# Kernel tuning notes

Hardware: AMD Instinct MI355X
Metric: run time of the kernel (lower is better)

Reference implementation:

```python
import jax, jax.numpy as jnp
import numpy as np

D_EMBED = 1024
D_HEAD = 128


def setup_inputs() -> dict:
    key = jax.random.key(0)
    kx, kq, kk, kv = jax.random.split(key, 4)
    x = jax.random.normal(kx, (4, 4096, D_EMBED), dtype=jnp.float32)
    # nn.Linear(d_embed, d_head, bias=False) weights, stored [out, in] like torch
    s = 1.0 / np.sqrt(D_EMBED)
    Wq = jax.random.uniform(kq, (D_HEAD, D_EMBED), jnp.float32, -s, s)
    Wk = jax.random.uniform(kk, (D_HEAD, D_EMBED), jnp.float32, -s, s)
    Wv = jax.random.uniform(kv, (D_HEAD, D_EMBED), jnp.float32, -s, s)
    return {"x": x, "Wq": Wq, "Wk": Wk, "Wv": Wv}


def reference(x, Wq, Wk, Wv):
    # q,k,v: [b, s, d_head]
    q = jnp.einsum("bse,he->bsh", x, Wq)
    k = jnp.einsum("bse,he->bsh", x, Wk)
    v = jnp.einsum("bse,he->bsh", x, Wv)
    # original: (q @ k^T) * d_head**-0.5, then divided by sqrt(d_embed)
    scale = 1.0 / (np.sqrt(D_HEAD) * np.sqrt(D_EMBED))
    scores = jnp.einsum("bqh,bkh->bqk", q, k) * jnp.float32(scale)  # [b, s, s]
    attn = jax.nn.softmax(scores, axis=-1)
    return jnp.einsum("bqk,bkh->bqh", attn, v)
```

## Files before the change

kernel.cpp:

```cpp
#include <hip/hip_runtime.h>
#include <stdint.h>

typedef __bf16 bf16x8 __attribute__((ext_vector_type(8)));
typedef float  f32x4  __attribute__((ext_vector_type(4)));

#define ATTN_SCALE 2.7621359e-3f

__device__ __forceinline__ unsigned short f2bf(float f) {
  union { float f; uint32_t u; } v; v.f = f;
  uint32_t u = v.u;
  uint32_t r = (u + 0x7FFFu + ((u >> 16) & 1u)) >> 16;
  return (unsigned short)r;
}

__device__ __forceinline__ void load_lds16(const unsigned short* g, unsigned short* l) {
  __builtin_amdgcn_global_load_lds(
      (const __attribute__((address_space(1))) void*)g,
      (__attribute__((address_space(3))) void*)l, 16, 0, 0);
}

__device__ __forceinline__ f32x4 mfma16(bf16x8 a, bf16x8 b, f32x4 c) {
  return __builtin_amdgcn_mfma_f32_16x16x32_bf16(a, b, c, 0, 0, 0);
}

__device__ __forceinline__ bf16x8 ones_bf16() {
  union { unsigned short u[8]; bf16x8 v; } c;
#pragma unroll
  for (int j = 0; j < 8; ++j) c.u[j] = 0x3F80;
  return c.v;
}

__global__ __launch_bounds__(256) void k_cvt(const float* __restrict__ src,
                                             unsigned short* __restrict__ dst, int n4) {
  int i = blockIdx.x * 256 + threadIdx.x;
  if (i >= n4) return;
  float4 f = ((const float4*)src)[i];
  ushort4 o;
  o.x = f2bf(f.x); o.y = f2bf(f.y); o.z = f2bf(f.z); o.w = f2bf(f.w);
  ((ushort4*)dst)[i] = o;
}

__global__ __launch_bounds__(256) void k_cvtw(const float* __restrict__ a,
                                              const float* __restrict__ b,
                                              const float* __restrict__ c,
                                              unsigned short* __restrict__ dst) {
  int i = blockIdx.x * 256 + threadIdx.x;
  int sel = i >> 15, off = i & 32767;
  const float* s = (sel == 0) ? a : (sel == 1) ? b : c;
  float4 f = ((const float4*)s)[off];
  ushort4 o;
  o.x = f2bf(f.x); o.y = f2bf(f.y); o.z = f2bf(f.z); o.w = f2bf(f.w);
  ((ushort4*)dst)[i] = o;
}

__global__ __launch_bounds__(256, 2) void k_proj(
    const unsigned short* __restrict__ X,
    const unsigned short* __restrict__ W,
    unsigned short* __restrict__ Qb,
    unsigned short* __restrict__ Kb,
    unsigned short* __restrict__ Vt)
{
  __shared__ __align__(16) unsigned short sm[128 * 32 * 2];
  unsigned short* As = sm;
  unsigned short* Bs = sm + 4096;
  const int t = threadIdx.x;
  const int mtile = blockIdx.x;
  const int nt = blockIdx.y;
  const int w = t >> 6, lane = t & 63, quad = lane >> 4, l15 = lane & 15;
  const int wm = w & 1, wn = w >> 1;

  const unsigned short* Wsel = W + nt * (128 * 1024);
  const unsigned short* Ag = X + (size_t)(mtile * 128) * 1024;

  const unsigned short* ag0 = Ag + (size_t)(t >> 2) * 1024 + (t & 3) * 8;
  const unsigned short* bg0 = Wsel + (size_t)(t >> 2) * 1024 + (t & 3) * 8;
  unsigned short* aw = &As[(t >> 6) * 512];
  unsigned short* bw = &Bs[(t >> 6) * 512];

  f32x4 acc[4][4] = {};

  for (int kt = 0; kt < 32; ++kt) {
    __syncthreads();
    const unsigned short* ak = ag0 + kt * 32;
    const unsigned short* bk = bg0 + kt * 32;
    load_lds16(ak,             aw);
    load_lds16(ak + 64 * 1024, aw + 2048);
    load_lds16(bk,             bw);
    load_lds16(bk + 64 * 1024, bw + 2048);
    __syncthreads();

    bf16x8 af[4], bfr[4];
#pragma unroll
    for (int i = 0; i < 4; ++i)
      af[i] = *(const bf16x8*)&As[(wm * 64 + i * 16 + l15) * 32 + quad * 8];
#pragma unroll
    for (int j = 0; j < 4; ++j)
      bfr[j] = *(const bf16x8*)&Bs[(wn * 64 + j * 16 + l15) * 32 + quad * 8];
#pragma unroll
    for (int i = 0; i < 4; ++i)
#pragma unroll
      for (int j = 0; j < 4; ++j)
        acc[i][j] = mfma16(af[i], bfr[j], acc[i][j]);
  }

  if (nt != 2) {
    const int m0 = mtile * 128 + wm * 64;
#pragma unroll
    for (int i = 0; i < 4; ++i)
#pragma unroll
      for (int j = 0; j < 4; ++j)
#pragma unroll
        for (int r = 0; r < 4; ++r) {
          int m = m0 + i * 16 + quad * 4 + r;
          int n = wn * 64 + j * 16 + l15;
          float v = acc[i][j][r];
          if (nt == 0) Qb[(size_t)m * 128 + n] = f2bf(v * ATTN_SCALE);
          else         Kb[(size_t)m * 128 + n] = f2bf(v);
        }
  } else {
    float* Ts = (float*)sm;
    const int bb = mtile >> 5;
    const int s0 = (mtile & 31) * 128;
#pragma unroll
    for (int jj = 0; jj < 8; ++jj) {
      __syncthreads();
      if (wn == (jj >> 2)) {
        const int j = jj & 3;
#pragma unroll
        for (int i = 0; i < 4; ++i)
#pragma unroll
          for (int r = 0; r < 4; ++r)
            Ts[(wm * 64 + i * 16 + quad * 4 + r) * 17 + l15] = acc[i][j][r];
      }
      __syncthreads();
      int n2 = jj * 16 + (t >> 4), m2 = (t & 15) * 8;
      union { unsigned short u[8]; uint4 v; } pk;
#pragma unroll
      for (int e = 0; e < 8; ++e) pk.u[e] = f2bf(Ts[(m2 + e) * 17 + (t >> 4)]);
      *(uint4*)&Vt[((size_t)(bb * 128 + n2)) * 4096 + s0 + m2] = pk.v;
    }
  }
}

__global__ __launch_bounds__(256, 2) void k_flash(
    const unsigned short* __restrict__ Qb,
    const unsigned short* __restrict__ Kb,
    const unsigned short* __restrict__ Vt,
    float* __restrict__ Om,
    float* __restrict__ lp)
{
  __shared__ __align__(16) unsigned short smem[8192 * 3 + 5120];
  unsigned short* Vsh = smem + 16384;
  unsigned short* Psh = smem + 24576;
  float* Ob  = (float*)smem;
  float* lsh = (float*)(smem + 24576);

  const int t = threadIdx.x;
  const int w = t >> 6, lane = t & 63, quad = lane >> 4, l15 = lane & 15;
  const int h = w & 1, p = w >> 1;
  const int qt = blockIdx.x, b = blockIdx.y, sp = blockIdx.z;

  const unsigned short* Qg = Qb + (size_t)(b * 4096 + qt * 64 + h * 32) * 128;
  const unsigned short* Kg = Kb + (size_t)b * 4096 * 128;
  const unsigned short* Vg = Vt + (size_t)b * 128 * 4096;

  bf16x8 qf[2][4];
#pragma unroll
  for (int mt = 0; mt < 2; ++mt)
#pragma unroll
    for (int kk = 0; kk < 4; ++kk)
      qf[mt][kk] = *(const bf16x8*)&Qg[(size_t)(mt * 16 + l15) * 128 + kk * 32 + quad * 8];

  f32x4 O[2][8] = {};
  f32x4 Ol[2] = {};

  const unsigned short* kg0 = Kg + (size_t)(t >> 4) * 128 + (((t & 15) ^ ((t >> 5) & 7)) * 8);
  const unsigned short* vg0 = Vg + (size_t)(t >> 3) * 4096 + (((t & 7) ^ ((t >> 3) & 7)) * 8);
  unsigned short* vw = &Vsh[w * 512];

  const int kt0 = sp * 32;

  {
    const unsigned short* kg = kg0 + (size_t)kt0 * 8192;
    unsigned short* kw = &smem[w * 512];
#pragma unroll
    for (int it = 0; it < 4; ++it)
      load_lds16(kg + it * 2048, kw + it * 2048);
  }

  for (int i = 0; i < 32; ++i) {
    const int cur = i & 1, nxt = cur ^ 1;
    __syncthreads();
    {
      const unsigned short* vg = vg0 + (size_t)(kt0 + i) * 64;
#pragma unroll
      for (int it = 0; it < 4; ++it)
        load_lds16(vg + (size_t)it * 131072, vw + it * 2048);
      const int ktn = (i < 31) ? (kt0 + i + 1) : kt0;
      const unsigned short* kg = kg0 + (size_t)ktn * 8192;
      unsigned short* kw = &smem[nxt * 8192 + w * 512];
#pragma unroll
      for (int it = 0; it < 4; ++it)
        load_lds16(kg + it * 2048, kw + it * 2048);
    }

    const unsigned short* Kshc = &smem[cur * 8192];
    f32x4 sc[2][2] = {};
#pragma unroll
    for (int ntk = 0; ntk < 2; ++ntk) {
      const int row = p * 32 + 2 * l15 + ntk;
#pragma unroll
      for (int kk = 0; kk < 4; ++kk) {
        bf16x8 kf = *(const bf16x8*)&Kshc[row * 128 + (((kk * 4 + quad) ^ (l15 & 7)) * 8)];
        sc[0][ntk] = mfma16(qf[0][kk], kf, sc[0][ntk]);
        sc[1][ntk] = mfma16(qf[1][kk], kf, sc[1][ntk]);
      }
    }

#pragma unroll
    for (int mt = 0; mt < 2; ++mt)
#pragma unroll
      for (int r = 0; r < 4; ++r) {
        float e0 = __expf(sc[mt][0][r]);
        float e1 = __expf(sc[mt][1][r]);
        int row = mt * 16 + quad * 4 + r;
        uint32_t pk = (uint32_t)f2bf(e0) | ((uint32_t)f2bf(e1) << 16);
        *(uint32_t*)&Psh[w * 1280 + row * 40 + 2 * l15] = pk;
      }

    asm volatile("s_waitcnt vmcnt(4) lgkmcnt(0)" ::: "memory");
    asm volatile("s_barrier" ::: "memory");

    bf16x8 pf0 = *(const bf16x8*)&Psh[w * 1280 + l15 * 40 + quad * 8];
    bf16x8 pf1 = *(const bf16x8*)&Psh[w * 1280 + (16 + l15) * 40 + quad * 8];
    const bf16x8 one = ones_bf16();
    Ol[0] = mfma16(pf0, one, Ol[0]);
    Ol[1] = mfma16(pf1, one, Ol[1]);
#pragma unroll
    for (int dt = 0; dt < 8; ++dt) {
      bf16x8 vf = *(const bf16x8*)&Vsh[(dt * 16 + l15) * 64 + (((p * 4 + quad) ^ (l15 & 7)) * 8)];
      O[0][dt] = mfma16(pf0, vf, O[0][dt]);
      O[1][dt] = mfma16(pf1, vf, O[1][dt]);
    }
  }

  __syncthreads();
  if (p == 1) {
#pragma unroll
    for (int mt = 0; mt < 2; ++mt)
#pragma unroll
      for (int r = 0; r < 4; ++r) {
        int row = h * 32 + mt * 16 + quad * 4 + r;
        if (l15 == 0) lsh[row] = Ol[mt][r];
#pragma unroll
        for (int dt = 0; dt < 8; ++dt)
          Ob[row * 128 + dt * 16 + l15] = O[mt][dt][r];
      }
  }
  __syncthreads();
  if (p == 0) {
    const size_t rowbase = (size_t)b * 4096 + qt * 64;
    float* Omp = Om + (size_t)sp * 2097152;
#pragma unroll
    for (int mt = 0; mt < 2; ++mt)
#pragma unroll
      for (int r = 0; r < 4; ++r) {
        int row = h * 32 + mt * 16 + quad * 4 + r;
#pragma unroll
        for (int dt = 0; dt < 8; ++dt)
          Omp[(rowbase + row) * 128 + dt * 16 + l15] =
              O[mt][dt][r] + Ob[row * 128 + dt * 16 + l15];
        if (l15 == 0)
          lp[(size_t)sp * 16384 + rowbase + row] = Ol[mt][r] + lsh[row];
      }
  }
}

__global__ __launch_bounds__(256) void k_merge(const float* __restrict__ Om,
                                               const float* __restrict__ lp,
                                               float* __restrict__ out) {
  int i = blockIdx.x * 256 + threadIdx.x;
  int row = i >> 5;
  float inv = 1.0f / (lp[row] + lp[16384 + row]);
  float4 a = ((const float4*)Om)[i];
  float4 c = ((const float4*)Om)[524288 + i];
  float4 o;
  o.x = (a.x + c.x) * inv;
  o.y = (a.y + c.y) * inv;
  o.z = (a.z + c.z) * inv;
  o.w = (a.w + c.w) * inv;
  ((float4*)out)[i] = o;
}

extern "C" void kernel_launch(void* const* d_in, const int* in_sizes, int n_in,
                              void* d_out, int out_size, void* d_ws, size_t ws_size,
                              hipStream_t stream) {
  const float* x  = (const float*)d_in[0];
  const float* Wq = (const float*)d_in[1];
  const float* Wk = (const float*)d_in[2];
  const float* Wv = (const float*)d_in[3];
  float* out = (float*)d_out;

  unsigned short* ws  = (unsigned short*)d_ws;
  unsigned short* xbf = ws;
  unsigned short* wbf = xbf + 16777216;
  unsigned short* Qb  = wbf + 393216;
  unsigned short* Kb  = Qb + 2097152;
  unsigned short* Vt  = Kb + 2097152;
  float* lp  = (float*)(Vt + 2097152);
  float* Om  = (float*)xbf;

  k_cvt<<<16384, 256, 0, stream>>>(x, xbf, 4194304);
  k_cvtw<<<384, 256, 0, stream>>>(Wq, Wk, Wv, wbf);
  k_proj<<<dim3(128, 3), 256, 0, stream>>>(xbf, wbf, Qb, Kb, Vt);
  k_flash<<<dim3(64, 4, 2), 256, 0, stream>>>(Qb, Kb, Vt, Om, lp);
  k_merge<<<2048, 256, 0, stream>>>(Om, lp, out);
}
```

Measured before the change: 179.4 us.

## Fuse x fp32-to-bf16 conversion into projection GEMM with smaller M tiles

Removes the standalone pass that converts x to bf16 and instead has the projection kernel load fp32 x directly, convert it in registers and store it to LDS. The M tile shrinks from 128 to 64 rows, which doubles the grid and raises the occupancy hint to 3. This avoids writing and re-reading a 32 MB bf16 copy of x. The cost is that each of the three projection column tiles now reads and converts fp32 x separately, the A load no longer goes through the direct global-to-LDS path, and the smaller tile gives less reuse per block.

```diff
diff --git a/kernel.cpp b/kernel.cpp
--- a/kernel.cpp
+++ b/kernel.cpp
@@ -28,16 +28,6 @@
 #pragma unroll
   for (int j = 0; j < 8; ++j) c.u[j] = 0x3F80;
   return c.v;
-}
-
-__global__ __launch_bounds__(256) void k_cvt(const float* __restrict__ src,
-                                             unsigned short* __restrict__ dst, int n4) {
-  int i = blockIdx.x * 256 + threadIdx.x;
-  if (i >= n4) return;
-  float4 f = ((const float4*)src)[i];
-  ushort4 o;
-  o.x = f2bf(f.x); o.y = f2bf(f.y); o.z = f2bf(f.z); o.w = f2bf(f.w);
-  ((ushort4*)dst)[i] = o;
 }
 
 __global__ __launch_bounds__(256) void k_cvtw(const float* __restrict__ a,
@@ -53,60 +43,61 @@
   ((ushort4*)dst)[i] = o;
 }
 
-__global__ __launch_bounds__(256, 2) void k_proj(
-    const unsigned short* __restrict__ X,
+__global__ __launch_bounds__(256, 3) void k_proj(
+    const float* __restrict__ X,
     const unsigned short* __restrict__ W,
     unsigned short* __restrict__ Qb,
     unsigned short* __restrict__ Kb,
     unsigned short* __restrict__ Vt)
 {
-  __shared__ __align__(16) unsigned short sm[128 * 32 * 2];
+  __shared__ __align__(16) unsigned short sm[2048 + 4096];
   unsigned short* As = sm;
-  unsigned short* Bs = sm + 4096;
+  unsigned short* Bs = sm + 2048;
   const int t = threadIdx.x;
   const int mtile = blockIdx.x;
   const int nt = blockIdx.y;
   const int w = t >> 6, lane = t & 63, quad = lane >> 4, l15 = lane & 15;
   const int wm = w & 1, wn = w >> 1;
 
-  const unsigned short* Wsel = W + nt * (128 * 1024);
-  const unsigned short* Ag = X + (size_t)(mtile * 128) * 1024;
-
-  const unsigned short* ag0 = Ag + (size_t)(t >> 2) * 1024 + (t & 3) * 8;
-  const unsigned short* bg0 = Wsel + (size_t)(t >> 2) * 1024 + (t & 3) * 8;
-  unsigned short* aw = &As[(t >> 6) * 512];
-  unsigned short* bw = &Bs[(t >> 6) * 512];
-
-  f32x4 acc[4][4] = {};
+  const float* ag0 = X + (size_t)(mtile * 64 + (t >> 2)) * 1024 + (t & 3) * 8;
+  const unsigned short* bg0 = W + (size_t)nt * 131072 + (size_t)(t >> 2) * 1024 + (t & 3) * 8;
+  unsigned short* aw = &As[(t >> 2) * 32 + (t & 3) * 8];
+  unsigned short* bw = &Bs[(t >> 2) * 32 + (t & 3) * 8];
+
+  f32x4 acc[2][4] = {};
 
   for (int kt = 0; kt < 32; ++kt) {
+    float4 a0 = *(const float4*)(ag0 + kt * 32);
+    float4 a1 = *(const float4*)(ag0 + kt * 32 + 4);
     __syncthreads();
-    const unsigned short* ak = ag0 + kt * 32;
-    const unsigned short* bk = bg0 + kt * 32;
-    load_lds16(ak,             aw);
-    load_lds16(ak + 64 * 1024, aw + 2048);
-    load_lds16(bk,             bw);
-    load_lds16(bk + 64 * 1024, bw + 2048);
+    load_lds16(bg0 + kt * 32,             bw);
+    load_lds16(bg0 + kt * 32 + 64 * 1024, bw + 2048);
+    union { unsigned short u[8]; uint4 v; } pa;
+    pa.u[0] = f2bf(a0.x); pa.u[1] = f2bf(a0.y);
+    pa.u[2] = f2bf(a0.z); pa.u[3] = f2bf(a0.w);
+    pa.u[4] = f2bf(a1.x); pa.u[5] = f2bf(a1.y);
+    pa.u[6] = f2bf(a1.z); pa.u[7] = f2bf(a1.w);
+    *(uint4*)aw = pa.v;
     __syncthreads();
 
-    bf16x8 af[4], bfr[4];
-#pragma unroll
-    for (int i = 0; i < 4; ++i)
-      af[i] = *(const bf16x8*)&As[(wm * 64 + i * 16 + l15) * 32 + quad * 8];
+    bf16x8 af[2], bfr[4];
+#pragma unroll
+    for (int i = 0; i < 2; ++i)
+      af[i] = *(const bf16x8*)&As[(wm * 32 + i * 16 + l15) * 32 + quad * 8];
 #pragma unroll
     for (int j = 0; j < 4; ++j)
       bfr[j] = *(const bf16x8*)&Bs[(wn * 64 + j * 16 + l15) * 32 + quad * 8];
 #pragma unroll
-    for (int i = 0; i < 4; ++i)
+    for (int i = 0; i < 2; ++i)
 #pragma unroll
       for (int j = 0; j < 4; ++j)
         acc[i][j] = mfma16(af[i], bfr[j], acc[i][j]);
   }
 
   if (nt != 2) {
-    const int m0 = mtile * 128 + wm * 64;
-#pragma unroll
-    for (int i = 0; i < 4; ++i)
+    const int m0 = mtile * 64 + wm * 32;
+#pragma unroll
+    for (int i = 0; i < 2; ++i)
 #pragma unroll
       for (int j = 0; j < 4; ++j)
 #pragma unroll
@@ -119,25 +110,26 @@
         }
   } else {
     float* Ts = (float*)sm;
-    const int bb = mtile >> 5;
-    const int s0 = (mtile & 31) * 128;
+    const int bb = mtile >> 6;
+    const int s0 = (mtile & 63) * 64;
 #pragma unroll
     for (int jj = 0; jj < 8; ++jj) {
       __syncthreads();
       if (wn == (jj >> 2)) {
         const int j = jj & 3;
 #pragma unroll
-        for (int i = 0; i < 4; ++i)
+        for (int i = 0; i < 2; ++i)
 #pragma unroll
           for (int r = 0; r < 4; ++r)
-            Ts[(wm * 64 + i * 16 + quad * 4 + r) * 17 + l15] = acc[i][j][r];
+            Ts[(wm * 32 + i * 16 + quad * 4 + r) * 17 + l15] = acc[i][j][r];
       }
       __syncthreads();
-      int n2 = jj * 16 + (t >> 4), m2 = (t & 15) * 8;
-      union { unsigned short u[8]; uint4 v; } pk;
-#pragma unroll
-      for (int e = 0; e < 8; ++e) pk.u[e] = f2bf(Ts[(m2 + e) * 17 + (t >> 4)]);
-      *(uint4*)&Vt[((size_t)(bb * 128 + n2)) * 4096 + s0 + m2] = pk.v;
+      int n2 = jj * 16 + (t >> 4);
+      int m2 = (t & 15) * 4;
+      union { unsigned short u[4]; uint2 v; } pk;
+#pragma unroll
+      for (int e = 0; e < 4; ++e) pk.u[e] = f2bf(Ts[(m2 + e) * 17 + (t >> 4)]);
+      *(uint2*)&Vt[((size_t)(bb * 128 + n2)) * 4096 + s0 + m2] = pk.v;
     }
   }
 }
@@ -302,17 +294,15 @@
   float* out = (float*)d_out;
 
   unsigned short* ws  = (unsigned short*)d_ws;
-  unsigned short* xbf = ws;
-  unsigned short* wbf = xbf + 16777216;
+  unsigned short* wbf = ws;
   unsigned short* Qb  = wbf + 393216;
   unsigned short* Kb  = Qb + 2097152;
   unsigned short* Vt  = Kb + 2097152;
-  float* lp  = (float*)(Vt + 2097152);
-  float* Om  = (float*)xbf;
-
-  k_cvt<<<16384, 256, 0, stream>>>(x, xbf, 4194304);
+  float* Om = (float*)(Vt + 2097152);
+  float* lp = Om + 4194304;
+
   k_cvtw<<<384, 256, 0, stream>>>(Wq, Wk, Wv, wbf);
-  k_proj<<<dim3(128, 3), 256, 0, stream>>>(xbf, wbf, Qb, Kb, Vt);
+  k_proj<<<dim3(256, 3), 256, 0, stream>>>(x, wbf, Qb, Kb, Vt);
   k_flash<<<dim3(64, 4, 2), 256, 0, stream>>>(Qb, Kb, Vt, Om, lp);
   k_merge<<<2048, 256, 0, stream>>>(Om, lp, out);
 }
```

Measured after the change: 179.2 us. Within noise of the previous version (-0.1%).
